# Kernel tuning notes

Measured on AMD Instinct MI355X. Metric: run time of the kernel, lower is better.

The kernel has to match this reference:

```python
import jax, jax.numpy as jnp
import numpy as np
import math

B, S, D, H = 2, 2048, 1024, 16
DK = D // H
SCALE = math.sqrt(DK)
NEG_BIG = -1e9


def setup_inputs() -> dict:
    key = jax.random.key(0)
    ks = jax.random.split(key, 7)
    x = jax.random.normal(ks[0], (B, S, D), dtype=jnp.float32)
    # additive causal mask: 0 on/below diagonal, -inf above
    causal = jnp.triu(jnp.ones((S, S), dtype=bool), k=1)
    mask = jnp.where(causal, -jnp.inf, 0.0).astype(jnp.float32)
    key_padding_mask = jax.random.bernoulli(ks[1], 0.1, (B, S))
    init = 1.0 / math.sqrt(D)
    Wq = jax.random.normal(ks[2], (D, D), dtype=jnp.float32) * init
    Wk = jax.random.normal(ks[3], (D, D), dtype=jnp.float32) * init
    Wv = jax.random.normal(ks[4], (D, D), dtype=jnp.float32) * init
    Wo = jax.random.normal(ks[5], (D, D), dtype=jnp.float32) * init
    bo = jnp.zeros((D,), dtype=jnp.float32)
    return {"x": x, "mask": mask, "key_padding_mask": key_padding_mask,
            "Wq": Wq, "Wk": Wk, "Wv": Wv, "Wo": Wo, "bo": bo}


def reference(x, mask, key_padding_mask, Wq, Wk, Wv, Wo, bo):
    b, s, d = x.shape
    # project and split heads -> [B,H,S,Dk]
    def heads(W):
        return jnp.einsum('bsd,de->bse', x, W).reshape(b, s, H, DK).transpose(0, 2, 1, 3)
    Q, K, V = heads(Wq), heads(Wk), heads(Wv)
    scores = jnp.einsum('bhqd,bhkd->bhqk', Q, K) / SCALE          # [B,H,S,S]
    scores = scores + mask[None, None]                            # additive attn mask
    scores = jnp.where(key_padding_mask[:, None, None, :], -jnp.inf, scores)
    # rows whose max is -inf (fully masked) get all scores set to -1e9
    max_scores = jnp.max(scores, axis=-1, keepdims=True)
    scores = jnp.where(jnp.isinf(max_scores), NEG_BIG, scores)
    attn = jax.nn.softmax(scores, axis=-1)
    attn = jnp.where(jnp.isnan(attn), 0.0, attn)
    # dropout is identity in eval mode
    ctx = jnp.einsum('bhqk,bhkd->bhqd', attn, V)                  # [B,H,S,Dk]
    ctx = ctx.transpose(0, 2, 1, 3).reshape(b, s, d)
    return jnp.einsum('bsd,de->bse', ctx, Wo) + bo
```

## Files before the change

kernel.cpp:

```cpp
#include <hip/hip_runtime.h>
#include <stdint.h>

#define NB 2
#define NS 2048
#define ND 1024
#define NH 16
#define NDK 64

typedef __attribute__((ext_vector_type(8))) short s8v;
typedef __attribute__((ext_vector_type(4))) float f4v;
typedef __attribute__((ext_vector_type(4))) unsigned short us4v;
typedef __attribute__((ext_vector_type(8))) unsigned short us8v;
typedef __attribute__((ext_vector_type(2))) uint32_t u2v;

__device__ __forceinline__ unsigned short f2bf(float f) {
  uint32_t u = __builtin_bit_cast(uint32_t, f);
  u = (u + 0x7fffu + ((u >> 16) & 1u)) >> 16;
  return (unsigned short)u;
}
__device__ __forceinline__ float bf2f(unsigned short h) {
  uint32_t u = ((uint32_t)h) << 16;
  return __builtin_bit_cast(float, u);
}
__device__ __forceinline__ uint32_t cvtpk(float lo, float hi) {
  uint32_t r;
  asm("v_cvt_pk_bf16_f32 %0, %1, %2" : "=v"(r) : "v"(lo), "v"(hi));
  return r;
}

__device__ __forceinline__ void gload16(const void* g, void* l) {
  __builtin_amdgcn_global_load_lds(
      (const __attribute__((address_space(1))) void*)g,
      (__attribute__((address_space(3))) void*)l, 16, 0, 0);
}

__global__ void k_convert_x(const float* __restrict__ x, unsigned short* __restrict__ xbf) {
  int i = (blockIdx.x * 256 + threadIdx.x) * 4;
  float4 v = *(const float4*)(x + i);
  us4v o;
  o[0] = f2bf(v.x); o[1] = f2bf(v.y); o[2] = f2bf(v.z); o[3] = f2bf(v.w);
  *(us4v*)(xbf + i) = o;
}

__global__ void k_transpose_w(const float* __restrict__ Wq, const float* __restrict__ Wk,
                              const float* __restrict__ Wv, const float* __restrict__ Wo,
                              unsigned short* __restrict__ wt_qkv, unsigned short* __restrict__ wt_o) {
  __shared__ float tls[64][65];
  int bid = blockIdx.x;
  int mat = bid >> 8;
  int tile = bid & 255;
  int tk = tile >> 4, tn = tile & 15;
  const float* W = (mat == 0) ? Wq : (mat == 1) ? Wk : (mat == 2) ? Wv : Wo;
  int t = threadIdx.x;
  int lr = t >> 2;
  int lc0 = (t & 3) * 16;
  const float* src = W + (size_t)(tk * 64 + lr) * 1024 + tn * 64 + lc0;
#pragma unroll
  for (int j = 0; j < 16; j += 4) {
    float4 v = *(const float4*)(src + j);
    tls[lr][lc0 + j + 0] = v.x; tls[lr][lc0 + j + 1] = v.y;
    tls[lr][lc0 + j + 2] = v.z; tls[lr][lc0 + j + 3] = v.w;
  }
  __syncthreads();
  float scale = (mat == 0) ? 0.125f : 1.0f;
  int nr = t >> 2, kc0 = (t & 3) * 16;
  unsigned short* dst = ((mat < 3) ? (wt_qkv + (size_t)(mat * 1024 + tn * 64 + nr) * 1024)
                                   : (wt_o + (size_t)(tn * 64 + nr) * 1024)) + tk * 64 + kc0;
  us8v o0, o1;
#pragma unroll
  for (int j = 0; j < 8; j++) o0[j] = f2bf(tls[kc0 + j][nr] * scale);
#pragma unroll
  for (int j = 0; j < 8; j++) o1[j] = f2bf(tls[kc0 + 8 + j][nr] * scale);
  *(us8v*)(dst) = o0;
  *(us8v*)(dst + 8) = o1;
}

template <int MODE>
__global__ __launch_bounds__(256) void k_gemm(const unsigned short* __restrict__ A,
                                              const unsigned short* __restrict__ Bt,
                                              unsigned short* __restrict__ qklin,
                                              unsigned short* __restrict__ vt,
                                              const float* __restrict__ bias,
                                              float* __restrict__ out) {
  __shared__ unsigned short lds_a[128 * 64];
  __shared__ unsigned short lds_b[128 * 64];
  const int K = 1024;
  int m0 = blockIdx.y * 128, n0 = blockIdx.x * 128;
  int tid = threadIdx.x, lane = tid & 63, w = tid >> 6;
  int wm = w >> 1, wn = w & 1;
  int g = lane >> 4, c0 = lane & 15;
  int rrel = lane >> 3;
  int gran = lane & 7;
  f4v acc[4][4];
#pragma unroll
  for (int mi = 0; mi < 4; mi++)
#pragma unroll
    for (int ni = 0; ni < 4; ni++) acc[mi][ni] = (f4v){0.f, 0.f, 0.f, 0.f};

  for (int kt = 0; kt < K / 64; ++kt) {
#pragma unroll
    for (int i = 0; i < 4; i++) {
      int r = 32 * w + 8 * i + rrel;
      gload16(A + (size_t)(m0 + r) * K + kt * 64 + 8 * (gran ^ rrel),
              (void*)(lds_a + (32 * w + 8 * i) * 64));
      gload16(Bt + (size_t)(n0 + r) * K + kt * 64 + 8 * (gran ^ rrel),
              (void*)(lds_b + (32 * w + 8 * i) * 64));
    }
    __syncthreads();
#pragma unroll
    for (int c = 0; c < 2; c++) {
      s8v af[4], bfr[4];
#pragma unroll
      for (int mi = 0; mi < 4; mi++) {
        int row = 64 * wm + 16 * mi + c0;
        af[mi] = *(const s8v*)(lds_a + row * 64 + 8 * ((g + 4 * c) ^ (c0 & 7)));
      }
#pragma unroll
      for (int ni = 0; ni < 4; ni++) {
        int row = 64 * wn + 16 * ni + c0;
        bfr[ni] = *(const s8v*)(lds_b + row * 64 + 8 * ((g + 4 * c) ^ (c0 & 7)));
      }
#pragma unroll
      for (int mi = 0; mi < 4; mi++)
#pragma unroll
        for (int ni = 0; ni < 4; ni++)
          acc[mi][ni] = __builtin_amdgcn_mfma_f32_16x16x32_bf16(af[mi], bfr[ni], acc[mi][ni], 0, 0, 0);
    }
    __syncthreads();
  }

#pragma unroll
  for (int mi = 0; mi < 4; mi++)
#pragma unroll
    for (int ni = 0; ni < 4; ni++)
#pragma unroll
      for (int r = 0; r < 4; r++) {
        int m = m0 + 64 * wm + 16 * mi + 4 * g + r;
        int n = n0 + 64 * wn + 16 * ni + c0;
        float v = acc[mi][ni][r];
        if (MODE == 0) {
          unsigned short hv = f2bf(v);
          if (n < 2048) {
            qklin[(size_t)m * 2048 + n] = hv;
          } else {
            int b = m >> 11, s = m & 2047;
            int hh = (n - 2048) >> 6, dk = n & 63;
            vt[(size_t)((b * 16 + hh) * 64 + dk) * 2048 + s] = hv;
          }
        } else {
          out[(size_t)m * 1024 + n] = v + bias[n];
        }
      }
}

__global__ void k_vmean(const unsigned short* __restrict__ vt, float* __restrict__ vmean) {
  int row = blockIdx.x * 4 + (threadIdx.x >> 6);
  int lane = threadIdx.x & 63;
  const unsigned short* p = vt + (size_t)row * 2048 + lane * 32;
  float s = 0.f;
#pragma unroll
  for (int j = 0; j < 32; j += 8) {
    us8v v = *(const us8v*)(p + j);
#pragma unroll
    for (int e = 0; e < 8; e++) s += bf2f(v[e]);
  }
#pragma unroll
  for (int m = 1; m < 64; m <<= 1) s += __shfl_xor(s, m);
  if (lane == 0) vmean[row] = s * (1.0f / 2048.0f);
}

__global__ __launch_bounds__(256) void k_attn(const unsigned short* __restrict__ qklin,
                                              const unsigned short* __restrict__ vt,
                                              const int* __restrict__ kpm,
                                              const float* __restrict__ vmean,
                                              unsigned short* __restrict__ ctx) {
  __shared__ unsigned short lds_k[2][64 * 64];
  __shared__ unsigned short lds_v[64 * 64];
  __shared__ unsigned short p_lds[4][16 * 64];
  int wg = blockIdx.x;
  int qt = 31 - (wg >> 5), bh = wg & 31;
  int b = bh >> 4, h = bh & 15;
  int tid = threadIdx.x, lane = tid & 63, w = tid >> 6;
  int g = lane >> 4, c0 = lane & 15;
  int q0 = qt * 64 + w * 16;
  unsigned short* pl = p_lds[w];
  int rrel = lane >> 3, gran = lane & 7;

  const unsigned short* ksrc0 = qklin + (size_t)(b * NS) * 2048 + 1024 + h * 64;
  const unsigned short* vsrc0 = vt + (size_t)(bh * 64) * 2048;

  const unsigned short* qbase = qklin + (size_t)(b * NS + q0 + c0) * 2048 + h * 64 + 8 * g;
  s8v qf0 = *(const s8v*)(qbase);
  s8v qf1 = *(const s8v*)(qbase + 32);

  f4v cacc[4];
#pragma unroll
  for (int d = 0; d < 4; d++) cacc[d] = (f4v){0.f, 0.f, 0.f, 0.f};
  float m_s = -1e30f, l_s = 0.f;
  int qrow = q0 + c0;

#pragma unroll
  for (int i = 0; i < 2; i++) {
    int r = 16 * w + 8 * i + rrel;
    gload16(ksrc0 + (size_t)r * 2048 + 8 * (gran ^ rrel),
            (void*)(lds_k[0] + (16 * w + 8 * i) * 64));
  }
  __syncthreads();

  int nkt = qt + 1;
  for (int it = 0; it < nkt; ++it) {
    int kb = it * 64;
    int cur = it & 1;
#pragma unroll
    for (int i = 0; i < 2; i++) {
      int r = 16 * w + 8 * i + rrel;
      gload16(vsrc0 + (size_t)r * 2048 + kb + 8 * (gran ^ rrel),
              (void*)(lds_v + (16 * w + 8 * i) * 64));
    }
    if (it < qt) {
#pragma unroll
      for (int i = 0; i < 2; i++) {
        int r = 16 * w + 8 * i + rrel;
        gload16(ksrc0 + (size_t)(kb + 64 + r) * 2048 + 8 * (gran ^ rrel),
                (void*)(lds_k[cur ^ 1] + (16 * w + 8 * i) * 64));
      }
    }
    int kp = kpm[b * NS + kb + lane];
    uint64_t padmask = __ballot(kp != 0);
    f4v sacc[4];
#pragma unroll
    for (int t = 0; t < 4; t++) {
      int row = 16 * t + c0;
      s8v kf0 = *(const s8v*)(lds_k[cur] + row * 64 + 8 * (g ^ (c0 & 7)));
      s8v kf1 = *(const s8v*)(lds_k[cur] + row * 64 + 8 * ((4 + g) ^ (c0 & 7)));
      f4v z = (f4v){0.f, 0.f, 0.f, 0.f};
      z = __builtin_amdgcn_mfma_f32_16x16x32_bf16(kf0, qf0, z, 0, 0, 0);
      z = __builtin_amdgcn_mfma_f32_16x16x32_bf16(kf1, qf1, z, 0, 0, 0);
      sacc[t] = z;
    }
    int thr = qrow - kb;
    uint64_t cmask = (thr >= 63) ? ~0ull : ((2ull << thr) - 1ull);
    uint64_t valid = cmask & ~padmask;
    float p[4][4];
    float mx = -1e30f;
#pragma unroll
    for (int t = 0; t < 4; t++) {
      uint32_t nib = (uint32_t)(valid >> (16 * t + 4 * g)) & 0xFu;
#pragma unroll
      for (int r = 0; r < 4; r++) {
        float s = sacc[t][r];
        s = ((nib >> r) & 1u) ? s : -1e30f;
        p[t][r] = s;
      }
      mx = fmaxf(mx, fmaxf(fmaxf(p[t][0], p[t][1]), fmaxf(p[t][2], p[t][3])));
    }
    mx = fmaxf(mx, __shfl_xor(mx, 16));
    mx = fmaxf(mx, __shfl_xor(mx, 32));
    float mnew = fmaxf(m_s, mx);
    float a = __expf(m_s - mnew);
    float rs = 0.f;
#pragma unroll
    for (int t = 0; t < 4; t++)
#pragma unroll
      for (int r = 0; r < 4; r++) {
        float e = __expf(p[t][r] - mnew);
        p[t][r] = e;
        rs += e;
      }
    rs += __shfl_xor(rs, 16);
    rs += __shfl_xor(rs, 32);
    rs = (mnew > -1e29f) ? rs : 0.f;
    l_s = l_s * a + rs;
    m_s = mnew;
    {
      int ybase = 20 * g;
#pragma unroll
      for (int r = 0; r < 4; r++) {
        float ar = __shfl(a, ybase + r);
#pragma unroll
        for (int d = 0; d < 4; d++) cacc[d][r] *= ar;
      }
    }
#pragma unroll
    for (int t = 0; t < 4; t++) {
      u2v pk;
      pk[0] = cvtpk(p[t][0], p[t][1]);
      pk[1] = cvtpk(p[t][2], p[t][3]);
      int gr = (2 * t + (g >> 1)) ^ (c0 & 7);
      *(u2v*)((char*)pl + c0 * 128 + gr * 16 + 8 * (g & 1)) = pk;
    }
    __syncthreads();
#pragma unroll
    for (int c = 0; c < 2; c++) {
      int off = c0 * 128 + 16 * g + 64 * c;
      off ^= (c0 & 7) << 4;
      s8v pf = *(const s8v*)((const char*)pl + off);
#pragma unroll
      for (int d = 0; d < 4; d++) {
        int row = 16 * d + c0;
        s8v vf = *(const s8v*)(lds_v + row * 64 + 8 * ((4 * c + g) ^ (c0 & 7)));
        cacc[d] = __builtin_amdgcn_mfma_f32_16x16x32_bf16(pf, vf, cacc[d], 0, 0, 0);
      }
    }
    __syncthreads();
  }
  float lq[4];
  {
    int ybase = 20 * g;
#pragma unroll
    for (int r = 0; r < 4; r++) lq[r] = __shfl(l_s, ybase + r);
  }
#pragma unroll
  for (int d = 0; d < 4; d++)
#pragma unroll
    for (int r = 0; r < 4; r++) {
      int q = q0 + 4 * g + r;
      float l = lq[r];
      float v = (l > 0.f) ? cacc[d][r] / l : vmean[bh * 64 + 16 * d + c0];
      ctx[(size_t)(b * NS + q) * ND + h * 64 + 16 * d + c0] = f2bf(v);
    }
}

extern "C" void kernel_launch(void* const* d_in, const int* in_sizes, int n_in,
                              void* d_out, int out_size, void* d_ws, size_t ws_size,
                              hipStream_t stream) {
  const float* x  = (const float*)d_in[0];
  const int* kpm  = (const int*)d_in[2];
  const float* Wq = (const float*)d_in[3];
  const float* Wk = (const float*)d_in[4];
  const float* Wv = (const float*)d_in[5];
  const float* Wo = (const float*)d_in[6];
  const float* bo = (const float*)d_in[7];

  char* ws = (char*)d_ws;
  unsigned short* xbf   = (unsigned short*)(ws);
  unsigned short* wtqkv = (unsigned short*)(ws + 8u * 1024 * 1024);
  unsigned short* wto   = (unsigned short*)(ws + 14u * 1024 * 1024);
  unsigned short* vt    = (unsigned short*)(ws + 16u * 1024 * 1024);
  float* vmean          = (float*)(ws + 24u * 1024 * 1024);
  unsigned short* ctx   = xbf;
  unsigned short* qklin = (unsigned short*)d_out;

  k_convert_x<<<4096, 256, 0, stream>>>(x, xbf);
  k_transpose_w<<<1024, 256, 0, stream>>>(Wq, Wk, Wv, Wo, wtqkv, wto);
  dim3 g0(24, 32);
  k_gemm<0><<<g0, 256, 0, stream>>>(xbf, wtqkv, qklin, vt, nullptr, nullptr);
  k_vmean<<<512, 256, 0, stream>>>(vt, vmean);
  k_attn<<<1024, 256, 0, stream>>>(qklin, vt, kpm, vmean, ctx);
  dim3 g1(8, 32);
  k_gemm<1><<<g1, 256, 0, stream>>>(ctx, wto, nullptr, nullptr, bo, (float*)d_out);
}
```

Baseline: 147.0 us.

## Double-buffer GEMM LDS tiles and swizzle block order across XCDs

```diff
diff --git a/kernel.cpp b/kernel.cpp
--- a/kernel.cpp
+++ b/kernel.cpp
@@ -81,11 +81,14 @@
                                               unsigned short* __restrict__ qklin,
                                               unsigned short* __restrict__ vt,
                                               const float* __restrict__ bias,
-                                              float* __restrict__ out) {
-  __shared__ unsigned short lds_a[128 * 64];
-  __shared__ unsigned short lds_b[128 * 64];
+                                              float* __restrict__ out, int ntx) {
+  __shared__ unsigned short lds_a[2][128 * 64];
+  __shared__ unsigned short lds_b[2][128 * 64];
   const int K = 1024;
-  int m0 = blockIdx.y * 128, n0 = blockIdx.x * 128;
+  int bid = blockIdx.x;
+  int qc = gridDim.x >> 3;
+  int swz = (bid & 7) * qc + (bid >> 3);
+  int m0 = (swz / ntx) * 128, n0 = (swz % ntx) * 128;
   int tid = threadIdx.x, lane = tid & 63, w = tid >> 6;
   int wm = w >> 1, wn = w & 1;
   int g = lane >> 4, c0 = lane & 15;
@@ -97,28 +100,40 @@
 #pragma unroll
     for (int ni = 0; ni < 4; ni++) acc[mi][ni] = (f4v){0.f, 0.f, 0.f, 0.f};
 
+#pragma unroll
+  for (int i = 0; i < 4; i++) {
+    int r = 32 * w + 8 * i + rrel;
+    gload16(A + (size_t)(m0 + r) * K + 8 * (gran ^ rrel),
+            (void*)(lds_a[0] + (32 * w + 8 * i) * 64));
+    gload16(Bt + (size_t)(n0 + r) * K + 8 * (gran ^ rrel),
+            (void*)(lds_b[0] + (32 * w + 8 * i) * 64));
+  }
+  __syncthreads();
+
   for (int kt = 0; kt < K / 64; ++kt) {
-#pragma unroll
-    for (int i = 0; i < 4; i++) {
-      int r = 32 * w + 8 * i + rrel;
-      gload16(A + (size_t)(m0 + r) * K + kt * 64 + 8 * (gran ^ rrel),
-              (void*)(lds_a + (32 * w + 8 * i) * 64));
-      gload16(Bt + (size_t)(n0 + r) * K + kt * 64 + 8 * (gran ^ rrel),
-              (void*)(lds_b + (32 * w + 8 * i) * 64));
-    }
-    __syncthreads();
+    int cur = kt & 1;
+    if (kt < K / 64 - 1) {
+#pragma unroll
+      for (int i = 0; i < 4; i++) {
+        int r = 32 * w + 8 * i + rrel;
+        gload16(A + (size_t)(m0 + r) * K + (kt + 1) * 64 + 8 * (gran ^ rrel),
+                (void*)(lds_a[cur ^ 1] + (32 * w + 8 * i) * 64));
+        gload16(Bt + (size_t)(n0 + r) * K + (kt + 1) * 64 + 8 * (gran ^ rrel),
+                (void*)(lds_b[cur ^ 1] + (32 * w + 8 * i) * 64));
+      }
+    }
 #pragma unroll
     for (int c = 0; c < 2; c++) {
       s8v af[4], bfr[4];
 #pragma unroll
       for (int mi = 0; mi < 4; mi++) {
         int row = 64 * wm + 16 * mi + c0;
-        af[mi] = *(const s8v*)(lds_a + row * 64 + 8 * ((g + 4 * c) ^ (c0 & 7)));
+        af[mi] = *(const s8v*)(lds_a[cur] + row * 64 + 8 * ((g + 4 * c) ^ (c0 & 7)));
       }
 #pragma unroll
       for (int ni = 0; ni < 4; ni++) {
         int row = 64 * wn + 16 * ni + c0;
-        bfr[ni] = *(const s8v*)(lds_b + row * 64 + 8 * ((g + 4 * c) ^ (c0 & 7)));
+        bfr[ni] = *(const s8v*)(lds_b[cur] + row * 64 + 8 * ((g + 4 * c) ^ (c0 & 7)));
       }
 #pragma unroll
       for (int mi = 0; mi < 4; mi++)
@@ -343,10 +358,8 @@
 
   k_convert_x<<<4096, 256, 0, stream>>>(x, xbf);
   k_transpose_w<<<1024, 256, 0, stream>>>(Wq, Wk, Wv, Wo, wtqkv, wto);
-  dim3 g0(24, 32);
-  k_gemm<0><<<g0, 256, 0, stream>>>(xbf, wtqkv, qklin, vt, nullptr, nullptr);
+  k_gemm<0><<<768, 256, 0, stream>>>(xbf, wtqkv, qklin, vt, nullptr, nullptr, 24);
   k_vmean<<<512, 256, 0, stream>>>(vt, vmean);
   k_attn<<<1024, 256, 0, stream>>>(qklin, vt, kpm, vmean, ctx);
-  dim3 g1(8, 32);
-  k_gemm<1><<<g1, 256, 0, stream>>>(ctx, wto, nullptr, nullptr, bo, (float*)d_out);
-}
+  k_gemm<1><<<256, 256, 0, stream>>>(ctx, wto, nullptr, nullptr, bo, (float*)d_out, 8);
+}
```

Measured after the change: 144.5 us. Within noise of the previous version (-1.7%).
